# Kernel optimization log

Hardware: AMD Instinct MI355X
Metric: run time of the kernel (lower is better)

## Reference

```python
import jax, jax.numpy as jnp
import numpy as np

N_NODES = 50000
N_FEAT = 128
DIM = 10
N_EDGES = 1600000
N_GRAPHS = 1000


def setup_inputs() -> dict:
    key = jax.random.key(0)
    ks = jax.random.split(key, 8)
    x = jax.random.normal(ks[0], (N_NODES, N_FEAT), dtype=jnp.float32)
    W1_l = jax.random.normal(ks[1], (DIM, N_FEAT), dtype=jnp.float32) * 0.1
    W1_r = jax.random.normal(ks[2], (DIM, N_FEAT), dtype=jnp.float32) * 0.1
    W2_l = jax.random.normal(ks[3], (DIM, DIM), dtype=jnp.float32) * 0.3
    W2_r = jax.random.normal(ks[4], (DIM, DIM), dtype=jnp.float32) * 0.3
    Wfc = jax.random.normal(ks[5], (1, DIM), dtype=jnp.float32) * 0.3
    edge_index = jax.random.randint(ks[6], (2, N_EDGES), 0, N_NODES, dtype=jnp.int64)
    batch = jnp.sort(jax.random.randint(ks[7], (N_NODES,), 0, N_GRAPHS, dtype=jnp.int64))
    return {"x": x, "W1_l": W1_l, "W1_r": W1_r, "W2_l": W2_l, "W2_r": W2_r,
            "Wfc": Wfc, "edge_index": edge_index, "batch": batch}


def _sage_conv(h, src, dst, deg_inv, Wl, Wr):
    # mean aggregation over incoming neighbors, then two bias-free linears
    agg = jax.ops.segment_sum(h[src], dst, num_segments=N_NODES)  # [N, F]
    agg = agg * deg_inv[:, None]
    return agg @ Wl.T + h @ Wr.T


def reference(x, W1_l, W1_r, W2_l, W2_r, Wfc, edge_index, batch):
    src, dst = edge_index[0], edge_index[1]
    # in-degree per destination node (mean denominator, clamped at 1 like PyG)
    deg = jax.ops.segment_sum(jnp.ones((src.shape[0],), x.dtype), dst, num_segments=N_NODES)
    deg_inv = 1.0 / jnp.maximum(deg, 1.0)

    h = jax.nn.relu(_sage_conv(x, src, dst, deg_inv, W1_l, W1_r))
    h = _sage_conv(h, src, dst, deg_inv, W2_l, W2_r)

    # global mean pool over graphs
    counts = jax.ops.segment_sum(jnp.ones((N_NODES,), x.dtype), batch, num_segments=N_GRAPHS)
    pooled = jax.ops.segment_sum(h, batch, num_segments=N_GRAPHS)
    pooled = pooled / jnp.maximum(counts, 1.0)[:, None]

    return jax.nn.sigmoid(pooled @ Wfc.T)  # [N_GRAPHS, 1]
```

## Files before the change

### kernel.cpp

```cpp
#include <hip/hip_runtime.h>
#include <hip/hip_bf16.h>
#include <math.h>

#define N_NODES  50000
#define N_FEAT   128
#define DIM      10
#define N_EDGES  1600000
#define N_GRAPHS 1000
#define PSTRIDE  16
#define CAP      80
#define BSH      8
#define NBUCK    196
#define BCAP     9216
#define ACHUNK   4096
#define ABLOCKS  ((N_EDGES + ACHUNK - 1) / ACHUNK)
#define PBLOCKS  ((N_NODES + 255) / 256)
#define SPLIT    8
#define GSLOTS   128

__device__ __forceinline__ float bf2f(unsigned short u) {
    union { unsigned int i; float f; } v;
    v.i = ((unsigned int)u) << 16;
    return v.f;
}

__device__ __forceinline__ float wload(const void* w, int fm, int i) {
    return fm ? ((const float*)w)[i] : bf2f(((const unsigned short*)w)[i]);
}

__device__ __forceinline__ int iload(const void* p, int im, long long pos) {
    return im ? (int)((const long long*)p)[pos] : ((const int*)p)[pos];
}

__global__ void detect_setup_kernel(
    const unsigned short* __restrict__ w1l, const unsigned int* __restrict__ ei32,
    const void* __restrict__ W2l, const void* __restrict__ W2r,
    const void* __restrict__ Wfc,
    int* __restrict__ fmode, int* __restrict__ imode,
    float* __restrict__ vl, float* __restrict__ vr,
    int* __restrict__ bcur, float* __restrict__ gsum, float* __restrict__ gcnt) {
    __shared__ int bigcnt, oddnz;
    if (threadIdx.x == 0) { bigcnt = 0; oddnz = 0; }
    __syncthreads();
    for (int i = threadIdx.x; i < DIM * N_FEAT; i += 256) {
        int expo = (w1l[i] >> 7) & 0xFF;
        if (expo >= 0x90) atomicAdd(&bigcnt, 1);
    }
    for (int i = threadIdx.x; i < 2048; i += 256) {
        if (ei32[2 * i + 1] != 0) atomicAdd(&oddnz, 1);
    }
    for (int i = threadIdx.x; i < NBUCK; i += 256) bcur[i] = 0;
    for (int i = threadIdx.x; i < N_GRAPHS; i += 256) { gsum[i] = 0.f; gcnt[i] = 0.f; }
    __syncthreads();
    int fm = (bigcnt >= 4) ? 1 : 0;
    if (threadIdx.x == 0) { *fmode = fm; *imode = (oddnz == 0) ? 1 : 0; }
    int j = threadIdx.x;
    if (j < DIM) {
        float al = 0.f, ar = 0.f;
        for (int i = 0; i < DIM; i++) {
            float w = wload(Wfc, fm, i);
            al += w * wload(W2l, fm, i * DIM + j);
            ar += w * wload(W2r, fm, i * DIM + j);
        }
        vl[j] = al;
        vr[j] = ar;
    } else if (j < 16) {
        vl[j] = 0.f;
        vr[j] = 0.f;
    }
}

#define ACCUM8(f0)                                                  \
    _Pragma("unroll")                                               \
    for (int d = 0; d < DIM; d++) {                                 \
        _Pragma("unroll")                                           \
        for (int k = 0; k < 8; k++) {                               \
            accl[d] += xf[k] * wl[d * N_FEAT + (f0) + k];           \
            accr[d] += xf[k] * wr[d * N_FEAT + (f0) + k];           \
        }                                                           \
    }

__global__ __launch_bounds__(256) void fusedA_kernel(
    const void* __restrict__ ei, const void* __restrict__ x,
    const void* __restrict__ W1l, const void* __restrict__ W1r,
    const int* __restrict__ fmode, const int* __restrict__ imode,
    int* __restrict__ bcur, unsigned int* __restrict__ bedges,
    float* __restrict__ p, float* __restrict__ q) {
    __shared__ union U {
        struct { unsigned int stage[ACHUNK]; int hcnt[NBUCK]; int hbase[NBUCK]; } a;
        struct { float wl[DIM * N_FEAT]; float wr[DIM * N_FEAT]; } b;
    } sh;

    if (blockIdx.x < ABLOCKS) {
        int im = *imode;
        for (int b = threadIdx.x; b < NBUCK; b += 256) sh.a.hcnt[b] = 0;
        __syncthreads();
        long long e0 = (long long)blockIdx.x * ACHUNK;
        int nE = (int)min((long long)ACHUNK, (long long)N_EDGES - e0);
        for (int i = threadIdx.x; i < nE; i += 256) {
            int s = iload(ei, im, e0 + i);
            int d = iload(ei, im, (long long)N_EDGES + e0 + i);
            sh.a.stage[i] = (unsigned)s | ((unsigned)(d & 255) << 16) | ((unsigned)(d >> BSH) << 24);
            atomicAdd(&sh.a.hcnt[d >> BSH], 1);
        }
        __syncthreads();
        for (int b = threadIdx.x; b < NBUCK; b += 256) {
            int c = sh.a.hcnt[b];
            sh.a.hbase[b] = c ? atomicAdd(&bcur[b], c) : 0;
            sh.a.hcnt[b] = 0;
        }
        __syncthreads();
        for (int i = threadIdx.x; i < nE; i += 256) {
            unsigned rec = sh.a.stage[i];
            int b = rec >> 24;
            int pos = sh.a.hbase[b] + atomicAdd(&sh.a.hcnt[b], 1);
            if (pos < BCAP) bedges[(size_t)b * BCAP + pos] = rec;
        }
    } else {
        int fm = *fmode;
        float* wl = sh.b.wl;
        float* wr = sh.b.wr;
        for (int i = threadIdx.x; i < DIM * N_FEAT; i += 256) {
            wl[i] = wload(W1l, fm, i);
            wr[i] = wload(W1r, fm, i);
        }
        __syncthreads();
        int n = (blockIdx.x - ABLOCKS) * 256 + threadIdx.x;
        if (n >= N_NODES) return;

        float accl[DIM], accr[DIM];
#pragma unroll
        for (int d = 0; d < DIM; d++) { accl[d] = 0.f; accr[d] = 0.f; }

        if (fm) {
            const float4* xr = reinterpret_cast<const float4*>((const float*)x + (size_t)n * N_FEAT);
            for (int fb = 0; fb < N_FEAT / 8; fb++) {
                float4 v0 = xr[2 * fb];
                float4 v1 = xr[2 * fb + 1];
                float xf[8] = {v0.x, v0.y, v0.z, v0.w, v1.x, v1.y, v1.z, v1.w};
                ACCUM8(fb * 8)
            }
        } else {
            const uint4* xr = reinterpret_cast<const uint4*>((const unsigned short*)x + (size_t)n * N_FEAT);
            for (int fb = 0; fb < N_FEAT / 8; fb++) {
                uint4 v = xr[fb];
                float xf[8];
                xf[0] = bf2f((unsigned short)(v.x & 0xffff)); xf[1] = bf2f((unsigned short)(v.x >> 16));
                xf[2] = bf2f((unsigned short)(v.y & 0xffff)); xf[3] = bf2f((unsigned short)(v.y >> 16));
                xf[4] = bf2f((unsigned short)(v.z & 0xffff)); xf[5] = bf2f((unsigned short)(v.z >> 16));
                xf[6] = bf2f((unsigned short)(v.w & 0xffff)); xf[7] = bf2f((unsigned short)(v.w >> 16));
                ACCUM8(fb * 8)
            }
        }
        float* pr = p + (size_t)n * PSTRIDE;
        float* qr = q + (size_t)n * PSTRIDE;
#pragma unroll
        for (int d = 0; d < DIM; d++) { pr[d] = accl[d]; qr[d] = accr[d]; }
#pragma unroll
        for (int d = DIM; d < PSTRIDE; d++) { pr[d] = 0.f; qr[d] = 0.f; }
    }
}

__global__ __launch_bounds__(1024) void binB_kernel(
    const int* __restrict__ bcur, const unsigned int* __restrict__ bedges,
    int* __restrict__ cnt, unsigned short* __restrict__ col) {
    __shared__ unsigned short lcol[256 * CAP];
    __shared__ int lcnt[256];
    int b = blockIdx.x;
    if (threadIdx.x < 256) lcnt[threadIdx.x] = 0;
    __syncthreads();
    int m = min(bcur[b], BCAP);
    const unsigned int* seg = bedges + (size_t)b * BCAP;
    for (int i = threadIdx.x; i < m; i += 1024) {
        unsigned rec = seg[i];
        int nidx = (rec >> 16) & 255;
        int pos = atomicAdd(&lcnt[nidx], 1);
        if (pos < CAP) lcol[nidx * CAP + pos] = (unsigned short)(rec & 0xffffu);
    }
    __syncthreads();
    int node0 = b << BSH;
    int nvalid = min(256, N_NODES - node0);
    if ((int)threadIdx.x < nvalid) cnt[node0 + threadIdx.x] = lcnt[threadIdx.x];
    int total = nvalid * CAP / 8;
    uint4* dst4 = (uint4*)(col + (size_t)node0 * CAP);
    const uint4* src4 = (const uint4*)lcol;
    for (int i = threadIdx.x; i < total; i += 1024) dst4[i] = src4[i];
}

__global__ __launch_bounds__(256) void pull1_kernel(
    const int* __restrict__ cnt, const unsigned short* __restrict__ col,
    const float* __restrict__ p, const float* __restrict__ q,
    const float* __restrict__ vl, const float* __restrict__ vr,
    float* __restrict__ t, float* __restrict__ u, float* __restrict__ dinv) {
    int g = blockIdx.x * 16 + (threadIdx.x >> 4);
    int sub = threadIdx.x & 15;
    if (g >= N_NODES) return;
    int deg = cnt[g];
    int dcl = min(deg, CAP);
    const unsigned short* cl = col + (size_t)g * CAP;
    float acc = 0.f;
    for (int k0 = 0; k0 < dcl; k0 += 8) {
        uint4 cv = *reinterpret_cast<const uint4*>(cl + k0);
        int cs[8];
        cs[0] = cv.x & 0xffff; cs[1] = cv.x >> 16;
        cs[2] = cv.y & 0xffff; cs[3] = cv.y >> 16;
        cs[4] = cv.z & 0xffff; cs[5] = cv.z >> 16;
        cs[6] = cv.w & 0xffff; cs[7] = cv.w >> 16;
#pragma unroll
        for (int j = 0; j < 8; j++) {
            float v = p[(size_t)cs[j] * PSTRIDE + sub];
            acc += (k0 + j < dcl) ? v : 0.f;
        }
    }
    float di = 1.0f / fmaxf((float)deg, 1.0f);
    float h = fmaxf(acc * di + q[(size_t)g * PSTRIDE + sub], 0.f);
    float tv = h * vl[sub];
    float uv = h * vr[sub];
#pragma unroll
    for (int off = 8; off > 0; off >>= 1) {
        tv += __shfl_xor(tv, off, 16);
        uv += __shfl_xor(uv, off, 16);
    }
    if (sub == 0) {
        t[g] = tv;
        u[g] = uv;
        dinv[g] = di;
    }
}

__global__ __launch_bounds__(256) void pull2B_kernel(
    const int* __restrict__ bcur, const unsigned int* __restrict__ bedges,
    const float* __restrict__ t, const float* __restrict__ u,
    const float* __restrict__ dinv, const void* __restrict__ batch,
    const int* __restrict__ imode,
    float* __restrict__ gsum, float* __restrict__ gcnt) {
    __shared__ float ldinv[256];
    __shared__ int   lb[256];
    __shared__ float lgs[GSLOTS];
    __shared__ float lgc[GSLOTS];
    int b = blockIdx.x / SPLIT;
    int s = blockIdx.x % SPLIT;
    int tid = threadIdx.x;
    int node0 = b << BSH;
    int nvalid = min(256, N_NODES - node0);
    int im = *imode;
    if (tid < nvalid) {
        ldinv[tid] = dinv[node0 + tid];
        lb[tid] = iload(batch, im, node0 + tid);
    }
    if (tid < GSLOTS) { lgs[tid] = 0.f; lgc[tid] = 0.f; }
    __syncthreads();
    int g0 = lb[0];
    int rng = lb[nvalid - 1] - g0 + 1;
    bool useLDS = (rng <= GSLOTS);
    int m = min(bcur[b], BCAP);
    int c0 = (m * s) / SPLIT, c1 = (m * (s + 1)) / SPLIT;
    const unsigned int* seg = bedges + (size_t)b * BCAP;
    for (int i = c0 + tid; i < c1; i += 256) {
        unsigned rec = seg[i];
        int src  = rec & 0xffffu;
        int nidx = (rec >> 16) & 255;
        float val = t[src] * ldinv[nidx];
        int gg = lb[nidx];
        if (useLDS) atomicAdd(&lgs[gg - g0], val);
        else        atomicAdd(gsum + gg, val);
    }
    if (s == 0 && tid < nvalid) {
        int gg = lb[tid];
        float uval = u[node0 + tid];
        if (useLDS) {
            atomicAdd(&lgs[gg - g0], uval);
            atomicAdd(&lgc[gg - g0], 1.0f);
        } else {
            atomicAdd(gsum + gg, uval);
            atomicAdd(gcnt + gg, 1.0f);
        }
    }
    __syncthreads();
    if (useLDS) {
        for (int i = tid; i < rng; i += 256) {
            float v = lgs[i];
            if (v != 0.f) atomicAdd(gsum + g0 + i, v);
            if (s == 0) {
                float c = lgc[i];
                if (c != 0.f) atomicAdd(gcnt + g0 + i, c);
            }
        }
    }
}

__global__ __launch_bounds__(256) void final_kernel(
    const float* __restrict__ gsum, const float* __restrict__ gcnt,
    const int* __restrict__ fmode, void* __restrict__ out) {
    int g = blockIdx.x * 256 + threadIdx.x;
    if (g >= N_GRAPHS) return;
    float pooled = gsum[g] / fmaxf(gcnt[g], 1.0f);
    float sg = 1.0f / (1.0f + expf(-pooled));
    if (*fmode) {
        ((float*)out)[g] = sg;
    } else {
        ((__hip_bfloat16*)out)[g] = __float2bfloat16(sg);
    }
}

extern "C" void kernel_launch(void* const* d_in, const int* in_sizes, int n_in,
                              void* d_out, int out_size, void* d_ws, size_t ws_size,
                              hipStream_t stream) {
    const void* x    = d_in[0];
    const void* W1l  = d_in[1];
    const void* W1r  = d_in[2];
    const void* W2l  = d_in[3];
    const void* W2r  = d_in[4];
    const void* Wfc  = d_in[5];
    const void* ei   = d_in[6];
    const void* batc = d_in[7];

    char* ws = (char*)d_ws;
    int*   fmode = (int*)ws;
    int*   imode = fmode + 1;
    float* vl   = (float*)(ws + 64);
    float* vr   = vl + 16;
    int*   bcur = (int*)(vr + 16);
    float* gsum = (float*)(bcur + NBUCK);
    float* gcnt = gsum + N_GRAPHS;
    unsigned int* bedges = (unsigned int*)(ws + ((((size_t)(gcnt + N_GRAPHS) - (size_t)ws) + 255) & ~(size_t)255));
    int*   cnt  = (int*)(bedges + (size_t)NBUCK * BCAP);
    unsigned short* col = (unsigned short*)(cnt + N_NODES);
    float* p    = (float*)(col + (size_t)N_NODES * CAP);
    float* q    = p + (size_t)N_NODES * PSTRIDE;
    float* t    = q + (size_t)N_NODES * PSTRIDE;
    float* u    = t + N_NODES;
    float* dinv = u + N_NODES;

    detect_setup_kernel<<<1, 256, 0, stream>>>(
        (const unsigned short*)W1l, (const unsigned int*)ei, W2l, W2r, Wfc,
        fmode, imode, vl, vr, bcur, gsum, gcnt);
    fusedA_kernel<<<ABLOCKS + PBLOCKS, 256, 0, stream>>>(
        ei, x, W1l, W1r, fmode, imode, bcur, bedges, p, q);
    binB_kernel<<<NBUCK, 1024, 0, stream>>>(bcur, bedges, cnt, col);
    pull1_kernel<<<(N_NODES * 16 + 255) / 256, 256, 0, stream>>>(cnt, col, p, q, vl, vr, t, u, dinv);
    pull2B_kernel<<<NBUCK * SPLIT, 256, 0, stream>>>(bcur, bedges, t, u, dinv, batc, imode, gsum, gcnt);
    final_kernel<<<(N_GRAPHS + 255) / 256, 256, 0, stream>>>(gsum, gcnt, fmode, d_out);
}
```

Baseline: 167.1 us.

## Fuse bucket CSR build into first-layer pull kernel via per-slice LDS binning

```diff
diff --git a/kernel.cpp b/kernel.cpp
--- a/kernel.cpp
+++ b/kernel.cpp
@@ -17,6 +17,8 @@
 #define PBLOCKS  ((N_NODES + 255) / 256)
 #define SPLIT    8
 #define GSLOTS   128
+#define SPLIT1   8
+#define SLICE    32
 
 __device__ __forceinline__ float bf2f(unsigned short u) {
     union { unsigned int i; float f; } v;
@@ -161,70 +163,68 @@
     }
 }
 
-__global__ __launch_bounds__(1024) void binB_kernel(
+__global__ __launch_bounds__(256) void pull1S_kernel(
     const int* __restrict__ bcur, const unsigned int* __restrict__ bedges,
-    int* __restrict__ cnt, unsigned short* __restrict__ col) {
-    __shared__ unsigned short lcol[256 * CAP];
-    __shared__ int lcnt[256];
-    int b = blockIdx.x;
-    if (threadIdx.x < 256) lcnt[threadIdx.x] = 0;
-    __syncthreads();
-    int m = min(bcur[b], BCAP);
-    const unsigned int* seg = bedges + (size_t)b * BCAP;
-    for (int i = threadIdx.x; i < m; i += 1024) {
-        unsigned rec = seg[i];
-        int nidx = (rec >> 16) & 255;
-        int pos = atomicAdd(&lcnt[nidx], 1);
-        if (pos < CAP) lcol[nidx * CAP + pos] = (unsigned short)(rec & 0xffffu);
-    }
-    __syncthreads();
-    int node0 = b << BSH;
-    int nvalid = min(256, N_NODES - node0);
-    if ((int)threadIdx.x < nvalid) cnt[node0 + threadIdx.x] = lcnt[threadIdx.x];
-    int total = nvalid * CAP / 8;
-    uint4* dst4 = (uint4*)(col + (size_t)node0 * CAP);
-    const uint4* src4 = (const uint4*)lcol;
-    for (int i = threadIdx.x; i < total; i += 1024) dst4[i] = src4[i];
-}
-
-__global__ __launch_bounds__(256) void pull1_kernel(
-    const int* __restrict__ cnt, const unsigned short* __restrict__ col,
     const float* __restrict__ p, const float* __restrict__ q,
     const float* __restrict__ vl, const float* __restrict__ vr,
     float* __restrict__ t, float* __restrict__ u, float* __restrict__ dinv) {
-    int g = blockIdx.x * 16 + (threadIdx.x >> 4);
-    int sub = threadIdx.x & 15;
-    if (g >= N_NODES) return;
-    int deg = cnt[g];
-    int dcl = min(deg, CAP);
-    const unsigned short* cl = col + (size_t)g * CAP;
-    float acc = 0.f;
-    for (int k0 = 0; k0 < dcl; k0 += 8) {
-        uint4 cv = *reinterpret_cast<const uint4*>(cl + k0);
-        int cs[8];
-        cs[0] = cv.x & 0xffff; cs[1] = cv.x >> 16;
-        cs[2] = cv.y & 0xffff; cs[3] = cv.y >> 16;
-        cs[4] = cv.z & 0xffff; cs[5] = cv.z >> 16;
-        cs[6] = cv.w & 0xffff; cs[7] = cv.w >> 16;
-#pragma unroll
-        for (int j = 0; j < 8; j++) {
-            float v = p[(size_t)cs[j] * PSTRIDE + sub];
-            acc += (k0 + j < dcl) ? v : 0.f;
-        }
-    }
-    float di = 1.0f / fmaxf((float)deg, 1.0f);
-    float h = fmaxf(acc * di + q[(size_t)g * PSTRIDE + sub], 0.f);
-    float tv = h * vl[sub];
-    float uv = h * vr[sub];
-#pragma unroll
-    for (int off = 8; off > 0; off >>= 1) {
-        tv += __shfl_xor(tv, off, 16);
-        uv += __shfl_xor(uv, off, 16);
-    }
-    if (sub == 0) {
-        t[g] = tv;
-        u[g] = uv;
-        dinv[g] = di;
+    __shared__ unsigned short lcol[SLICE * CAP];
+    __shared__ int lcnt[SLICE];
+    __shared__ float svl[16], svr[16];
+    int b = blockIdx.x / SPLIT1;
+    int s = blockIdx.x % SPLIT1;
+    int tid = threadIdx.x;
+    if (tid < SLICE) lcnt[tid] = 0;
+    if (tid < 16) { svl[tid] = vl[tid]; svr[tid] = vr[tid]; }
+    __syncthreads();
+    int m = min(bcur[b], BCAP);
+    const unsigned int* seg = bedges + (size_t)b * BCAP;
+    for (int i = tid; i < m; i += 256) {
+        unsigned rec = seg[i];
+        int nidx = (rec >> 16) & 255;
+        if ((nidx >> 5) == s) {
+            int nl = nidx & 31;
+            int pos = atomicAdd(&lcnt[nl], 1);
+            if (pos < CAP) lcol[nl * CAP + pos] = (unsigned short)(rec & 0xffffu);
+        }
+    }
+    __syncthreads();
+    int sub = tid & 15;
+    int grp = tid >> 4;
+    int node0 = (b << BSH) + s * SLICE;
+#pragma unroll
+    for (int it = 0; it < SLICE / 16; it++) {
+        int nl = it * 16 + grp;
+        int n = node0 + nl;
+        if (n < N_NODES) {
+            int deg = lcnt[nl];
+            int dcl = min(deg, CAP);
+            const unsigned short* cl = lcol + nl * CAP;
+            float acc = 0.f;
+            for (int k0 = 0; k0 < dcl; k0 += 8) {
+                uint4 cv = *reinterpret_cast<const uint4*>(cl + k0);
+                int cs[8];
+                cs[0] = cv.x & 0xffff; cs[1] = cv.x >> 16;
+                cs[2] = cv.y & 0xffff; cs[3] = cv.y >> 16;
+                cs[4] = cv.z & 0xffff; cs[5] = cv.z >> 16;
+                cs[6] = cv.w & 0xffff; cs[7] = cv.w >> 16;
+#pragma unroll
+                for (int j = 0; j < 8; j++) {
+                    float v = p[(size_t)cs[j] * PSTRIDE + sub];
+                    acc += (k0 + j < dcl) ? v : 0.f;
+                }
+            }
+            float di = 1.0f / fmaxf((float)deg, 1.0f);
+            float h = fmaxf(acc * di + q[(size_t)n * PSTRIDE + sub], 0.f);
+            float tv = h * svl[sub];
+            float uv = h * svr[sub];
+#pragma unroll
+            for (int off = 8; off > 0; off >>= 1) {
+                tv += __shfl_xor(tv, off, 16);
+                uv += __shfl_xor(uv, off, 16);
+            }
+            if (sub == 0) { t[n] = tv; u[n] = uv; dinv[n] = di; }
+        }
     }
 }
 
@@ -324,9 +324,7 @@
     float* gsum = (float*)(bcur + NBUCK);
     float* gcnt = gsum + N_GRAPHS;
     unsigned int* bedges = (unsigned int*)(ws + ((((size_t)(gcnt + N_GRAPHS) - (size_t)ws) + 255) & ~(size_t)255));
-    int*   cnt  = (int*)(bedges + (size_t)NBUCK * BCAP);
-    unsigned short* col = (unsigned short*)(cnt + N_NODES);
-    float* p    = (float*)(col + (size_t)N_NODES * CAP);
+    float* p    = (float*)(bedges + (size_t)NBUCK * BCAP);
     float* q    = p + (size_t)N_NODES * PSTRIDE;
     float* t    = q + (size_t)N_NODES * PSTRIDE;
     float* u    = t + N_NODES;
@@ -337,8 +335,7 @@
         fmode, imode, vl, vr, bcur, gsum, gcnt);
     fusedA_kernel<<<ABLOCKS + PBLOCKS, 256, 0, stream>>>(
         ei, x, W1l, W1r, fmode, imode, bcur, bedges, p, q);
-    binB_kernel<<<NBUCK, 1024, 0, stream>>>(bcur, bedges, cnt, col);
-    pull1_kernel<<<(N_NODES * 16 + 255) / 256, 256, 0, stream>>>(cnt, col, p, q, vl, vr, t, u, dinv);
+    pull1S_kernel<<<NBUCK * SPLIT1, 256, 0, stream>>>(bcur, bedges, p, q, vl, vr, t, u, dinv);
     pull2B_kernel<<<NBUCK * SPLIT, 256, 0, stream>>>(bcur, bedges, t, u, dinv, batc, imode, gsum, gcnt);
     final_kernel<<<(N_GRAPHS + 255) / 256, 256, 0, stream>>>(gsum, gcnt, fmode, d_out);
 }
```

Result: slower. 171.9 us (+2.9%).
